# Performance work log

Measured on AMD Instinct MI355X. Metric: run time of the kernel, lower is better.

## Reference

```python
import jax, jax.numpy as jnp
import numpy as np

D_MODEL = 512
NUM_HEADS = 8
HEAD_DIM = D_MODEL // NUM_HEADS  # 64
EMBEDDING_DIM = 512  # undefined global EmbeddingDim in source -> d_model
EVENT_DIM = 388      # undefined global EventDim in source -> MIDI event vocab
B, T = 2, 2048


def setup_inputs() -> dict:
    key = jax.random.key(0)
    ks = jax.random.split(key, 12)
    sc = 0.02
    v = jax.random.normal(ks[0], (B, T, D_MODEL), jnp.float32)
    k = jax.random.normal(ks[1], (B, T, D_MODEL), jnp.float32)
    q = jax.random.normal(ks[2], (B, T, D_MODEL), jnp.float32)
    mask = jnp.tril(jnp.ones((T, T), jnp.float32))  # causal mask, broadcasts to [H,B,T,T]
    Wq = jax.random.normal(ks[3], (D_MODEL, HEAD_DIM), jnp.float32) * sc
    bq = jnp.zeros((HEAD_DIM,), jnp.float32)
    Wk = jax.random.normal(ks[4], (D_MODEL, HEAD_DIM), jnp.float32) * sc
    bk = jnp.zeros((HEAD_DIM,), jnp.float32)
    Wv = jax.random.normal(ks[5], (D_MODEL, HEAD_DIM), jnp.float32) * sc
    bv = jnp.zeros((HEAD_DIM,), jnp.float32)
    E = jax.random.normal(ks[6], (NUM_HEADS, T, HEAD_DIM), jnp.float32) * sc
    Wo = jax.random.normal(ks[7], (D_MODEL, EMBEDDING_DIM), jnp.float32) * sc
    bo = jnp.zeros((EMBEDDING_DIM,), jnp.float32)
    Wl = jax.random.normal(ks[8], (EMBEDDING_DIM, EVENT_DIM), jnp.float32) * sc
    bl = jnp.zeros((EVENT_DIM,), jnp.float32)
    return {"v": v, "k": k, "q": q, "mask": mask, "Wq": Wq, "bq": bq,
            "Wk": Wk, "bk": bk, "Wv": Wv, "bv": bv, "E": E,
            "Wo": Wo, "bo": bo, "Wl": Wl, "bl": bl}


def _skew(S):
    # S: [H,B,T,T] -> Music-Transformer skew via left-pad, reshape, slice
    H, Bb, Tt, _ = S.shape
    S = jnp.pad(S, ((0, 0), (0, 0), (0, 0), (1, 0)))          # [H,B,T,T+1]
    S = S.reshape(H, Bb, Tt + 1, Tt)                           # [H,B,T+1,T]
    return S[:, :, 1:]                                         # [H,B,T,T]


def reference(v, k, q, mask, Wq, bq, Wk, bk, Wv, bv, E, Wo, bo, Wl, bl):
    # The source applies the SAME Dense per head, so all heads share q/k/v projections
    qh = q @ Wq + bq  # [B,T,hd]
    kh = k @ Wk + bk  # [B,T,hd]
    vh = v @ Wv + bv  # [B,T,hd]
    # relative-position scores per head: Q @ E^T then skew
    S = jnp.einsum('btd,hsd->hbts', qh, E)  # [H,B,T,T]
    S = _skew(S)
    qk = jnp.einsum('btd,bsd->bts', qh, kh)  # [B,T,T], identical across heads
    attn = (qk[None] + S) / np.sqrt(HEAD_DIM)  # [H,B,T,T]
    attn = attn * mask - jnp.asarray(1e10, attn.dtype) * (1.0 - mask)
    score = jax.nn.softmax(attn, axis=-1)
    ctx = jnp.einsum('hbts,bsd->hbtd', score, vh)  # [H,B,T,hd]
    ctx = jnp.transpose(ctx, (1, 2, 0, 3)).reshape(ctx.shape[1], ctx.shape[2], -1)  # [B,T,d_model]
    ctx = jax.nn.relu(ctx @ Wo + bo)  # [B,T,EmbeddingDim]
    logits = ctx @ Wl + bl            # [B,T,EventDim]
    return logits
```

## Files before the change

### kernel.cpp

```cpp
#include <hip/hip_runtime.h>
#include <hip/hip_bf16.h>


#define B_ 2
#define T_ 2048
#define DM_ 512
#define H_ 8
#define HD_ 64
#define ED_ 512
#define EV_ 388
#define BT_ (B_ * T_)

typedef __attribute__((ext_vector_type(8))) short short8;
typedef __attribute__((ext_vector_type(4))) float floatx4;

#define MFMA(a, b, c) __builtin_amdgcn_mfma_f32_16x16x32_bf16((a), (b), (c), 0, 0, 0)

__device__ __forceinline__ float bfs(unsigned short s) {
  union { unsigned int i; float f; } v; v.i = ((unsigned int)s) << 16; return v.f;
}
__device__ __forceinline__ unsigned short f2bf(float f) {
  __hip_bfloat16 h = __float2bfloat16(f);
  union { __hip_bfloat16 h; unsigned short u; } v; v.h = h; return v.u;
}
__device__ __forceinline__ float ldf(const void* p, int i, bool isbf) {
  return isbf ? bfs(((const unsigned short*)p)[i]) : ((const float*)p)[i];
}
__device__ __forceinline__ bool det_bf(const unsigned int* mask) {
  return mask[0] != 0x3F800000u;
}

__global__ __launch_bounds__(256) void prep_kernel(
    const void* __restrict__ E, const void* __restrict__ Wq,
    const void* __restrict__ Wk, const void* __restrict__ Wv,
    const void* __restrict__ Wo, const void* __restrict__ Wl,
    const unsigned int* __restrict__ mask,
    unsigned short* __restrict__ E_c, unsigned short* __restrict__ WqT,
    unsigned short* __restrict__ WkT, unsigned short* __restrict__ WvT,
    unsigned short* __restrict__ WoT, unsigned short* __restrict__ WlT) {
  const bool isbf = det_bf(mask);
  const int tid = threadIdx.x;
  int bi = blockIdx.x;
  if (bi < 1024) {
    const int i0 = (bi * 256 + tid) * 4;
    if (isbf) {
      *(uint2*)&E_c[i0] = *(const uint2*)((const unsigned short*)E + i0);
    } else {
      float4 f = *(const float4*)((const float*)E + i0);
      unsigned short p[4] = {f2bf(f.x), f2bf(f.y), f2bf(f.z), f2bf(f.w)};
      *(uint2*)&E_c[i0] = *(uint2*)p;
    }
    return;
  }
  bi -= 1024;
  const void* src; unsigned short* dst; int N, nb;
  if (bi < 16)       { src = Wq; dst = WqT; N = 64;  nb = bi; }
  else if (bi < 32)  { src = Wk; dst = WkT; N = 64;  nb = bi - 16; }
  else if (bi < 48)  { src = Wv; dst = WvT; N = 64;  nb = bi - 32; }
  else if (bi < 176) { src = Wo; dst = WoT; N = 512; nb = bi - 48; }
  else               { src = Wl; dst = WlT; N = 388; nb = bi - 176; }
  const int n = nb * 4 + (tid >> 6);
  const int k0 = (tid & 63) * 8;
  unsigned short vv[8];
#pragma unroll
  for (int j = 0; j < 8; ++j) {
    if (n >= N) vv[j] = 0;
    else if (isbf) vv[j] = ((const unsigned short*)src)[(size_t)(k0 + j) * N + n];
    else vv[j] = f2bf(((const float*)src)[(size_t)(k0 + j) * N + n]);
  }
  *(uint4*)&dst[(size_t)n * DM_ + k0] = *(uint4*)vv;
}

__global__ __launch_bounds__(256) void gemm_proj(
    const void* __restrict__ xq, const void* __restrict__ xk,
    const void* __restrict__ xv,
    const unsigned short* __restrict__ WqT, const unsigned short* __restrict__ WkT,
    const unsigned short* __restrict__ WvT,
    const void* __restrict__ bq, const void* __restrict__ bk,
    const void* __restrict__ bv, const unsigned int* __restrict__ mask,
    unsigned short* __restrict__ oq, unsigned short* __restrict__ ok,
    unsigned short* __restrict__ ovt) {
  __shared__ __align__(16) short sA[64][72];
  __shared__ __align__(16) short sW[64][72];
  const int sel = blockIdx.y;
  const void* x = (sel == 0) ? xq : (sel == 1) ? xk : xv;
  const unsigned short* WT = (sel == 0) ? WqT : (sel == 1) ? WkT : WvT;
  const void* bias = (sel == 0) ? bq : (sel == 1) ? bk : bv;
  const bool isbf = det_bf(mask);

  const int tid = threadIdx.x;
  const int w = tid >> 6, lane = tid & 63;
  const int q_ = lane >> 4, n_ = lane & 15;
  const int row0 = blockIdx.x * 64;

  floatx4 acc[4];
#pragma unroll
  for (int j = 0; j < 4; ++j) acc[j] = (floatx4){0.f, 0.f, 0.f, 0.f};

  for (int k0 = 0; k0 < DM_; k0 += 64) {
    if (isbf) {
#pragma unroll
      for (int it = 0; it < 2; ++it) {
        int idx = tid + it * 256;
        int rr = idx >> 3, cc = (idx & 7) * 8;
        *(uint4*)&sA[rr][cc] =
            *(const uint4*)((const unsigned short*)x + (size_t)(row0 + rr) * DM_ + k0 + cc);
      }
    } else {
#pragma unroll
      for (int it = 0; it < 4; ++it) {
        int idx = tid + it * 256;
        int rr = idx >> 4, cc = (idx & 15) * 4;
        float4 f = *(const float4*)((const float*)x + (size_t)(row0 + rr) * DM_ + k0 + cc);
        unsigned short p[4] = {f2bf(f.x), f2bf(f.y), f2bf(f.z), f2bf(f.w)};
        *(uint2*)&sA[rr][cc] = *(uint2*)p;
      }
    }
#pragma unroll
    for (int it = 0; it < 2; ++it) {
      int idx = tid + it * 256;
      int rr = idx >> 3, cc = (idx & 7) * 8;
      *(uint4*)&sW[rr][cc] = *(const uint4*)(WT + (size_t)rr * DM_ + k0 + cc);
    }
    __syncthreads();
    short8 a0 = *(const short8*)&sA[16 * w + n_][8 * q_];
    short8 a1 = *(const short8*)&sA[16 * w + n_][32 + 8 * q_];
#pragma unroll
    for (int nb = 0; nb < 4; ++nb) {
      short8 b0 = *(const short8*)&sW[16 * nb + n_][8 * q_];
      short8 b1 = *(const short8*)&sW[16 * nb + n_][32 + 8 * q_];
      acc[nb] = MFMA(a0, b0, acc[nb]);
      acc[nb] = MFMA(a1, b1, acc[nb]);
    }
    __syncthreads();
  }

#pragma unroll
  for (int nb = 0; nb < 4; ++nb) {
    const int col = 16 * nb + n_;
    const float bb = ldf(bias, col, isbf);
#pragma unroll
    for (int r = 0; r < 4; ++r) {
      int row = row0 + 16 * w + 4 * q_ + r;
      unsigned short val = f2bf(acc[nb][r] + bb);
      if (sel < 2) {
        unsigned short* o = (sel == 0) ? oq : ok;
        o[(size_t)row * HD_ + col] = val;
      } else {
        int b = row >> 11, s = row & 2047;
        ovt[(((size_t)(b * HD_ + col)) << 11) + s] = val;
      }
    }
  }
}

__device__ __forceinline__ int pbase_of(int ti) {
  return (ti < 16) ? (ti - 8) * 2 : (ti < 24) ? 16 + (ti - 16) * 3
                                              : 40 + (ti - 24) * 4;
}

__global__ __launch_bounds__(256) void attn_kernel(
    const unsigned short* __restrict__ qh, const unsigned short* __restrict__ kh,
    const unsigned short* __restrict__ vt, const unsigned short* __restrict__ E,
    unsigned short* __restrict__ ctxo, float* __restrict__ pc,
    float* __restrict__ ml) {
  __shared__ __align__(16) short sK[64][72];
  __shared__ __align__(16) short sVT[64][72];
  __shared__ __align__(16) short sP[64][72];

  const int id = blockIdx.x;
  const int hb = id / 80;
  const int rem = id % 80;
  int ti, c, nc;
  if (rem < 8)       { ti = rem;                 c = 0;            nc = 1; }
  else if (rem < 24) { ti = 8 + ((rem - 8) >> 1);  c = (rem - 8) & 1;  nc = 2; }
  else if (rem < 48) { ti = 16 + (rem - 24) / 3;   c = (rem - 24) % 3; nc = 3; }
  else               { ti = 24 + ((rem - 48) >> 2); c = (rem - 48) & 3; nc = 4; }
  const int nsteps = ti + 1;
  const int klo = (c * nsteps) / nc;
  const int khi = ((c + 1) * nsteps) / nc;

  const int h = hb >> 1, b = hb & 1;
  const int t0 = ti * 64;

  const int tid = threadIdx.x;
  const int w = tid >> 6, lane = tid & 63;
  const int q_ = lane >> 4, n_ = lane & 15;

  const int trow = t0 + 16 * w + n_;
  const unsigned short* qp = qh + (((size_t)((b << 11) + trow)) << 6) + (q_ << 3);
  const short8 qa0 = *(const short8*)qp;
  const short8 qa1 = *(const short8*)(qp + 32);

  short8 onesf;
#pragma unroll
  for (int j = 0; j < 8; ++j) onesf[j] = (short)0x3F80;

  floatx4 ctxa[4];
#pragma unroll
  for (int nb = 0; nb < 4; ++nb) ctxa[nb] = (floatx4){0.f, 0.f, 0.f, 0.f};
  floatx4 lacc = (floatx4){0.f, 0.f, 0.f, 0.f};

  const unsigned short* eb = E + ((size_t)h << 17);
  const unsigned short* kbase = kh + (((size_t)(b << 11)) << 6);
  const unsigned short* vbase = vt + (((size_t)(b << 6)) << 11);
  const int rrS = tid >> 3, ccS = (tid & 7) * 8;

  for (int kt = klo; kt < khi; ++kt) {
    const int s0 = kt * 64;
    const int rb = (T_ - 64) + s0 - t0;

    short8 e0[5], e1[5];
#pragma unroll
    for (int f = 0; f < 5; ++f) {
      int gr = rb + 16 * (3 - w + f) + n_;
      if (gr > T_ - 1) gr = T_ - 1;
      const unsigned short* ep = eb + ((size_t)gr << 6) + (q_ << 3);
      e0[f] = *(const short8*)ep;
      e1[f] = *(const short8*)(ep + 32);
    }

    __syncthreads();
#pragma unroll
    for (int it = 0; it < 2; ++it) {
      int rr = rrS + it * 32;
      *(uint4*)&sK[rr][ccS] =
          *(const uint4*)(kbase + (((size_t)(s0 + rr)) << 6) + ccS);
      *(uint4*)&sVT[rr][ccS] =
          *(const uint4*)(vbase + (((size_t)rr) << 11) + s0 + ccS);
    }
    __syncthreads();

    floatx4 qk[4];
#pragma unroll
    for (int nb = 0; nb < 4; ++nb) {
      short8 kb0 = *(const short8*)&sK[16 * nb + n_][8 * q_];
      short8 kb1 = *(const short8*)&sK[16 * nb + n_][32 + 8 * q_];
      qk[nb] = (floatx4){0.f, 0.f, 0.f, 0.f};
      qk[nb] = MFMA(qa0, kb0, qk[nb]);
      qk[nb] = MFMA(qa1, kb1, qk[nb]);
    }
    floatx4 qe[5];
#pragma unroll
    for (int f = 0; f < 5; ++f) {
      qe[f] = (floatx4){0.f, 0.f, 0.f, 0.f};
      qe[f] = MFMA(qa0, e0[f], qe[f]);
      qe[f] = MFMA(qa1, e1[f], qe[f]);
    }

    const bool diag = (kt == ti);
#pragma unroll
    for (int r = 0; r < 4; ++r) {
      const int t = 4 * q_ + r;
      const int ba = ((q_ << 4) | ((n_ - t + 15) & 15)) << 2;
      const int nd = (n_ + t + 1) & 15;
      const bool hi = nd > t;
#pragma unroll
      for (int mb = 0; mb < 4; ++mb) {
        float merged = hi ? qe[mb + 1][r] : qe[mb][r];
        float g = __int_as_float(
            __builtin_amdgcn_ds_bpermute(ba, __float_as_int(merged)));
        float sv = (qk[mb][r] + g) * 0.125f;
        if (diag && (16 * mb + n_ > 16 * w + t)) sv = -1.0e30f;
        sP[16 * w + t][16 * mb + n_] = (short)f2bf(__expf(sv));
      }
    }

    short8 pa0 = *(const short8*)&sP[16 * w + n_][8 * q_];
    short8 pa1 = *(const short8*)&sP[16 * w + n_][32 + 8 * q_];
#pragma unroll
    for (int nb = 0; nb < 4; ++nb) {
      short8 v0 = *(const short8*)&sVT[16 * nb + n_][8 * q_];
      short8 v1 = *(const short8*)&sVT[16 * nb + n_][32 + 8 * q_];
      ctxa[nb] = MFMA(pa0, v0, ctxa[nb]);
      ctxa[nb] = MFMA(pa1, v1, ctxa[nb]);
    }
    lacc = MFMA(pa0, onesf, lacc);
    lacc = MFMA(pa1, onesf, lacc);
  }

  if (nc == 1) {
#pragma unroll
    for (int r = 0; r < 4; ++r) {
      const float inv = 1.0f / lacc[r];
      const int row = t0 + 16 * w + 4 * q_ + r;
      const size_t base = (((size_t)((b << 11) + row)) << 9) + (h << 6) + n_;
#pragma unroll
      for (int nb = 0; nb < 4; ++nb)
        ctxo[base + 16 * nb] = f2bf(ctxa[nb][r] * inv);
    }
  } else {
    const int idx = hb * 72 + pbase_of(ti) + c;
    float* pcb = pc + ((size_t)idx << 12);
    float* mlb = ml + ((size_t)idx << 6);
#pragma unroll
    for (int r = 0; r < 4; ++r) {
      const int row = 16 * w + 4 * q_ + r;
#pragma unroll
      for (int nb = 0; nb < 4; ++nb)
        pcb[(row << 6) + 16 * nb + n_] = ctxa[nb][r];
      if (n_ == 0) mlb[row] = lacc[r];
    }
  }
}

__global__ __launch_bounds__(256) void combine_kernel(
    const float* __restrict__ pc, const float* __restrict__ ml,
    unsigned short* __restrict__ ctxo) {
  const int cb = blockIdx.x;
  const int hb = cb / 24;
  const int ti = 8 + cb % 24;
  const int nc = (ti >> 3) + 1;
  const int h = hb >> 1, b = hb & 1, t0 = ti * 64;
  const int tid = threadIdx.x;
  const int row = tid >> 2, seg = (tid & 3) * 16;
  const int idx0 = hb * 72 + pbase_of(ti);

  float lsum = 0.f;
  float4 a4[4];
#pragma unroll
  for (int j = 0; j < 4; ++j) a4[j] = (float4){0.f, 0.f, 0.f, 0.f};
  for (int c = 0; c < nc; ++c) {
    const int idx = idx0 + c;
    lsum += ml[((size_t)idx << 6) + row];
    const float* cp = pc + ((size_t)idx << 12) + (row << 6) + seg;
#pragma unroll
    for (int j = 0; j < 4; ++j) {
      float4 x = *(const float4*)(cp + 4 * j);
      a4[j].x += x.x; a4[j].y += x.y; a4[j].z += x.z; a4[j].w += x.w;
    }
  }
  const float inv = 1.0f / lsum;
  unsigned short o[16];
#pragma unroll
  for (int j = 0; j < 4; ++j) {
    o[4 * j + 0] = f2bf(a4[j].x * inv);
    o[4 * j + 1] = f2bf(a4[j].y * inv);
    o[4 * j + 2] = f2bf(a4[j].z * inv);
    o[4 * j + 3] = f2bf(a4[j].w * inv);
  }
  unsigned short* dst =
      ctxo + (((size_t)((b << 11) + t0 + row)) << 9) + (h << 6) + seg;
  *(uint4*)dst = *(uint4*)&o[0];
  *(uint4*)(dst + 8) = *(uint4*)&o[8];
}

template <int RELU>
__global__ __launch_bounds__(256) void mlp_mfma(
    const unsigned short* __restrict__ A, const unsigned short* __restrict__ WT,
    const void* __restrict__ bias, unsigned short* __restrict__ outBF,
    void* __restrict__ outD, const unsigned int* __restrict__ mask) {
  __shared__ __align__(16) short sA[64][72];
  __shared__ __align__(16) short sW[64][72];
  const int tid = threadIdx.x;
  const int w = tid >> 6, lane = tid & 63;
  const int q_ = lane >> 4, n_ = lane & 15;
  const int row0 = blockIdx.x * 64;
  const int n0 = blockIdx.y * 64;
  const bool isbf = det_bf(mask);

  floatx4 acc[4];
#pragma unroll
  for (int j = 0; j < 4; ++j) acc[j] = (floatx4){0.f, 0.f, 0.f, 0.f};

  for (int k0 = 0; k0 < DM_; k0 += 64) {
#pragma unroll
    for (int it = 0; it < 2; ++it) {
      int idx = tid + it * 256;
      int rr = idx >> 3, cc = (idx & 7) * 8;
      *(uint4*)&sA[rr][cc] = *(const uint4*)(A + (size_t)(row0 + rr) * DM_ + k0 + cc);
      *(uint4*)&sW[rr][cc] = *(const uint4*)(WT + (size_t)(n0 + rr) * DM_ + k0 + cc);
    }
    __syncthreads();
    short8 a0 = *(const short8*)&sA[16 * w + n_][8 * q_];
    short8 a1 = *(const short8*)&sA[16 * w + n_][32 + 8 * q_];
#pragma unroll
    for (int nb = 0; nb < 4; ++nb) {
      short8 b0 = *(const short8*)&sW[16 * nb + n_][8 * q_];
      short8 b1 = *(const short8*)&sW[16 * nb + n_][32 + 8 * q_];
      acc[nb] = MFMA(a0, b0, acc[nb]);
      acc[nb] = MFMA(a1, b1, acc[nb]);
    }
    __syncthreads();
  }

#pragma unroll
  for (int nb = 0; nb < 4; ++nb) {
    const int col = n0 + 16 * nb + n_;
    float bb = 0.f;
    if (RELU || col < EV_) bb = ldf(bias, col, isbf);
#pragma unroll
    for (int r = 0; r < 4; ++r) {
      const int row = row0 + 16 * w + 4 * q_ + r;
      float v = acc[nb][r] + bb;
      if (RELU) {
        outBF[(size_t)row * ED_ + col] = f2bf(fmaxf(v, 0.f));
      } else if (col < EV_) {
        if (isbf) ((unsigned short*)outD)[(size_t)row * EV_ + col] = f2bf(v);
        else      ((float*)outD)[(size_t)row * EV_ + col] = v;
      }
    }
  }
}

extern "C" void kernel_launch(void* const* d_in, const int* in_sizes, int n_in,
                              void* d_out, int out_size, void* d_ws, size_t ws_size,
                              hipStream_t stream) {
  const void* v  = d_in[0];
  const void* k  = d_in[1];
  const void* q  = d_in[2];
  const unsigned int* mask = (const unsigned int*)d_in[3];
  const void* Wq = d_in[4];
  const void* bq = d_in[5];
  const void* Wk = d_in[6];
  const void* bk = d_in[7];
  const void* Wv = d_in[8];
  const void* bv = d_in[9];
  const void* E  = d_in[10];
  const void* Wo = d_in[11];
  const void* bo = d_in[12];
  const void* Wl = d_in[13];
  const void* bl = d_in[14];

  char* p = (char*)d_ws;
  unsigned short* E_c  = (unsigned short*)p; p += (size_t)H_ * T_ * HD_ * 2;
  unsigned short* qhb  = (unsigned short*)p; p += (size_t)BT_ * HD_ * 2;
  unsigned short* khb  = (unsigned short*)p; p += (size_t)BT_ * HD_ * 2;
  unsigned short* vtb  = (unsigned short*)p; p += (size_t)BT_ * HD_ * 2;
  unsigned short* WqT  = (unsigned short*)p; p += (size_t)HD_ * DM_ * 2;
  unsigned short* WkT  = (unsigned short*)p; p += (size_t)HD_ * DM_ * 2;
  unsigned short* WvT  = (unsigned short*)p; p += (size_t)HD_ * DM_ * 2;
  unsigned short* WoT  = (unsigned short*)p; p += (size_t)ED_ * DM_ * 2;
  unsigned short* WlT  = (unsigned short*)p; p += (size_t)448 * DM_ * 2;
  unsigned short* ctxb = (unsigned short*)p; p += (size_t)BT_ * DM_ * 2;
  unsigned short* h1b  = (unsigned short*)p; p += (size_t)BT_ * ED_ * 2;
  float* pc = (float*)p; p += (size_t)16 * 72 * 4096 * 4;
  float* ml = (float*)p; p += (size_t)16 * 72 * 64 * 4;

  prep_kernel<<<dim3(1312), 256, 0, stream>>>(
      E, Wq, Wk, Wv, Wo, Wl, mask, E_c, WqT, WkT, WvT, WoT, WlT);
  gemm_proj<<<dim3(BT_ / 64, 3), 256, 0, stream>>>(
      q, k, v, WqT, WkT, WvT, bq, bk, bv, mask, qhb, khb, vtb);
  attn_kernel<<<dim3(1280), 256, 0, stream>>>(qhb, khb, vtb, E_c, ctxb, pc, ml);
  combine_kernel<<<dim3(384), 256, 0, stream>>>(pc, ml, ctxb);
  mlp_mfma<1><<<dim3(BT_ / 64, ED_ / 64), 256, 0, stream>>>(
      ctxb, WoT, bo, h1b, nullptr, mask);
  mlp_mfma<0><<<dim3(BT_ / 64, 448 / 64), 256, 0, stream>>>(
      h1b, WlT, bl, nullptr, d_out, mask);
}
```

Baseline: 225.0 us.

## Double-buffer K/V tiles in attention and fold split-KV combine via atomic counter

The attention loop now prefetches the next K/V tile into registers while computing on the current one, using double-buffered shared memory to hide global load latency. The separate combine kernel is removed: each split block bumps an atomic counter, and the last block to finish for a query tile reduces the partial results and writes the context. The counters are zeroed inside the projection kernel. This saves one kernel launch and overlaps memory with compute, at the cost of more shared memory, more register pressure and extra fences and atomics.

```diff
diff --git a/kernel.cpp b/kernel.cpp
--- a/kernel.cpp
+++ b/kernel.cpp
@@ -79,16 +79,19 @@
     const void* __restrict__ bq, const void* __restrict__ bk,
     const void* __restrict__ bv, const unsigned int* __restrict__ mask,
     unsigned short* __restrict__ oq, unsigned short* __restrict__ ok,
-    unsigned short* __restrict__ ovt) {
+    unsigned short* __restrict__ ovt, int* __restrict__ cnt) {
   __shared__ __align__(16) short sA[64][72];
   __shared__ __align__(16) short sW[64][72];
+  const int tid = threadIdx.x;
+  if (blockIdx.x == 0 && blockIdx.y == 0 && tid < 128) {
+    cnt[tid] = 0; cnt[tid + 128] = 0; cnt[tid + 256] = 0;
+  }
   const int sel = blockIdx.y;
   const void* x = (sel == 0) ? xq : (sel == 1) ? xk : xv;
   const unsigned short* WT = (sel == 0) ? WqT : (sel == 1) ? WkT : WvT;
   const void* bias = (sel == 0) ? bq : (sel == 1) ? bk : bv;
   const bool isbf = det_bf(mask);
 
-  const int tid = threadIdx.x;
   const int w = tid >> 6, lane = tid & 63;
   const int q_ = lane >> 4, n_ = lane & 15;
   const int row0 = blockIdx.x * 64;
@@ -163,16 +166,17 @@
     const unsigned short* __restrict__ qh, const unsigned short* __restrict__ kh,
     const unsigned short* __restrict__ vt, const unsigned short* __restrict__ E,
     unsigned short* __restrict__ ctxo, float* __restrict__ pc,
-    float* __restrict__ ml) {
-  __shared__ __align__(16) short sK[64][72];
-  __shared__ __align__(16) short sVT[64][72];
+    float* __restrict__ ml, int* __restrict__ cnt) {
+  __shared__ __align__(16) short sK[2][64][72];
+  __shared__ __align__(16) short sVT[2][64][72];
   __shared__ __align__(16) short sP[64][72];
+  __shared__ int lastFlag;
 
   const int id = blockIdx.x;
   const int hb = id / 80;
   const int rem = id % 80;
   int ti, c, nc;
-  if (rem < 8)       { ti = rem;                 c = 0;            nc = 1; }
+  if (rem < 8)       { ti = rem;                  c = 0;             nc = 1; }
   else if (rem < 24) { ti = 8 + ((rem - 8) >> 1);  c = (rem - 8) & 1;  nc = 2; }
   else if (rem < 48) { ti = 16 + (rem - 24) / 3;   c = (rem - 24) % 3; nc = 3; }
   else               { ti = 24 + ((rem - 48) >> 2); c = (rem - 48) & 3; nc = 4; }
@@ -206,9 +210,32 @@
   const unsigned short* vbase = vt + (((size_t)(b << 6)) << 11);
   const int rrS = tid >> 3, ccS = (tid & 7) * 8;
 
+  uint4 pk[2], pv[2];
+#define LOADKV(KT)                                                            \
+  {                                                                           \
+    const int s0p = (KT) * 64;                                                \
+    _Pragma("unroll")                                                         \
+    for (int it = 0; it < 2; ++it) {                                          \
+      int rr = rrS + it * 32;                                                 \
+      pk[it] = *(const uint4*)(kbase + (((size_t)(s0p + rr)) << 6) + ccS);    \
+      pv[it] = *(const uint4*)(vbase + (((size_t)rr) << 11) + s0p + ccS);     \
+    }                                                                         \
+  }
+
+  LOADKV(klo);
+#pragma unroll
+  for (int it = 0; it < 2; ++it) {
+    int rr = rrS + it * 32;
+    *(uint4*)&sK[0][rr][ccS] = pk[it];
+    *(uint4*)&sVT[0][rr][ccS] = pv[it];
+  }
+  __syncthreads();
+
+  int cur = 0;
   for (int kt = klo; kt < khi; ++kt) {
     const int s0 = kt * 64;
     const int rb = (T_ - 64) + s0 - t0;
+    const bool hasNext = (kt + 1 < khi);
 
     short8 e0[5], e1[5];
 #pragma unroll
@@ -219,23 +246,13 @@
       e0[f] = *(const short8*)ep;
       e1[f] = *(const short8*)(ep + 32);
     }
-
-    __syncthreads();
-#pragma unroll
-    for (int it = 0; it < 2; ++it) {
-      int rr = rrS + it * 32;
-      *(uint4*)&sK[rr][ccS] =
-          *(const uint4*)(kbase + (((size_t)(s0 + rr)) << 6) + ccS);
-      *(uint4*)&sVT[rr][ccS] =
-          *(const uint4*)(vbase + (((size_t)rr) << 11) + s0 + ccS);
-    }
-    __syncthreads();
+    if (hasNext) LOADKV(kt + 1);
 
     floatx4 qk[4];
 #pragma unroll
     for (int nb = 0; nb < 4; ++nb) {
-      short8 kb0 = *(const short8*)&sK[16 * nb + n_][8 * q_];
-      short8 kb1 = *(const short8*)&sK[16 * nb + n_][32 + 8 * q_];
+      short8 kb0 = *(const short8*)&sK[cur][16 * nb + n_][8 * q_];
+      short8 kb1 = *(const short8*)&sK[cur][16 * nb + n_][32 + 8 * q_];
       qk[nb] = (floatx4){0.f, 0.f, 0.f, 0.f};
       qk[nb] = MFMA(qa0, kb0, qk[nb]);
       qk[nb] = MFMA(qa1, kb1, qk[nb]);
@@ -270,14 +287,27 @@
     short8 pa1 = *(const short8*)&sP[16 * w + n_][32 + 8 * q_];
 #pragma unroll
     for (int nb = 0; nb < 4; ++nb) {
-      short8 v0 = *(const short8*)&sVT[16 * nb + n_][8 * q_];
-      short8 v1 = *(const short8*)&sVT[16 * nb + n_][32 + 8 * q_];
+      short8 v0 = *(const short8*)&sVT[cur][16 * nb + n_][8 * q_];
+      short8 v1 = *(const short8*)&sVT[cur][16 * nb + n_][32 + 8 * q_];
       ctxa[nb] = MFMA(pa0, v0, ctxa[nb]);
       ctxa[nb] = MFMA(pa1, v1, ctxa[nb]);
     }
     lacc = MFMA(pa0, onesf, lacc);
     lacc = MFMA(pa1, onesf, lacc);
-  }
+
+    if (hasNext) {
+      __syncthreads();
+#pragma unroll
+      for (int it = 0; it < 2; ++it) {
+        int rr = rrS + it * 32;
+        *(uint4*)&sK[cur ^ 1][rr][ccS] = pk[it];
+        *(uint4*)&sVT[cur ^ 1][rr][ccS] = pv[it];
+      }
+      __syncthreads();
+      cur ^= 1;
+    }
+  }
+#undef LOADKV
 
   if (nc == 1) {
 #pragma unroll
@@ -301,48 +331,45 @@
         pcb[(row << 6) + 16 * nb + n_] = ctxa[nb][r];
       if (n_ == 0) mlb[row] = lacc[r];
     }
-  }
-}
-
-__global__ __launch_bounds__(256) void combine_kernel(
-    const float* __restrict__ pc, const float* __restrict__ ml,
-    unsigned short* __restrict__ ctxo) {
-  const int cb = blockIdx.x;
-  const int hb = cb / 24;
-  const int ti = 8 + cb % 24;
-  const int nc = (ti >> 3) + 1;
-  const int h = hb >> 1, b = hb & 1, t0 = ti * 64;
-  const int tid = threadIdx.x;
-  const int row = tid >> 2, seg = (tid & 3) * 16;
-  const int idx0 = hb * 72 + pbase_of(ti);
-
-  float lsum = 0.f;
-  float4 a4[4];
-#pragma unroll
-  for (int j = 0; j < 4; ++j) a4[j] = (float4){0.f, 0.f, 0.f, 0.f};
-  for (int c = 0; c < nc; ++c) {
-    const int idx = idx0 + c;
-    lsum += ml[((size_t)idx << 6) + row];
-    const float* cp = pc + ((size_t)idx << 12) + (row << 6) + seg;
-#pragma unroll
-    for (int j = 0; j < 4; ++j) {
-      float4 x = *(const float4*)(cp + 4 * j);
-      a4[j].x += x.x; a4[j].y += x.y; a4[j].z += x.z; a4[j].w += x.w;
-    }
-  }
-  const float inv = 1.0f / lsum;
-  unsigned short o[16];
-#pragma unroll
-  for (int j = 0; j < 4; ++j) {
-    o[4 * j + 0] = f2bf(a4[j].x * inv);
-    o[4 * j + 1] = f2bf(a4[j].y * inv);
-    o[4 * j + 2] = f2bf(a4[j].z * inv);
-    o[4 * j + 3] = f2bf(a4[j].w * inv);
-  }
-  unsigned short* dst =
-      ctxo + (((size_t)((b << 11) + t0 + row)) << 9) + (h << 6) + seg;
-  *(uint4*)dst = *(uint4*)&o[0];
-  *(uint4*)(dst + 8) = *(uint4*)&o[8];
+    __threadfence();
+    if (tid == 0) {
+      int old = atomicAdd(&cnt[hb * 24 + (ti - 8)], 1);
+      lastFlag = (old == nc - 1) ? 1 : 0;
+    }
+    __syncthreads();
+    if (lastFlag) {
+      __threadfence();
+      const int row = tid >> 2, seg = (tid & 3) * 16;
+      const int idx0 = hb * 72 + pbase_of(ti);
+      float lsum = 0.f;
+      float4 a4[4];
+#pragma unroll
+      for (int j = 0; j < 4; ++j) a4[j] = (float4){0.f, 0.f, 0.f, 0.f};
+      for (int c2 = 0; c2 < nc; ++c2) {
+        const int ix = idx0 + c2;
+        lsum += ml[((size_t)ix << 6) + row];
+        const float* cp = pc + ((size_t)ix << 12) + (row << 6) + seg;
+#pragma unroll
+        for (int j = 0; j < 4; ++j) {
+          float4 x = *(const float4*)(cp + 4 * j);
+          a4[j].x += x.x; a4[j].y += x.y; a4[j].z += x.z; a4[j].w += x.w;
+        }
+      }
+      const float inv = 1.0f / lsum;
+      unsigned short o[16];
+#pragma unroll
+      for (int j = 0; j < 4; ++j) {
+        o[4 * j + 0] = f2bf(a4[j].x * inv);
+        o[4 * j + 1] = f2bf(a4[j].y * inv);
+        o[4 * j + 2] = f2bf(a4[j].z * inv);
+        o[4 * j + 3] = f2bf(a4[j].w * inv);
+      }
+      unsigned short* dst =
+          ctxo + (((size_t)((b << 11) + t0 + row)) << 9) + (h << 6) + seg;
+      *(uint4*)dst = *(uint4*)&o[0];
+      *(uint4*)(dst + 8) = *(uint4*)&o[8];
+    }
+  }
 }
 
 template <int RELU>
@@ -436,13 +463,14 @@
   unsigned short* h1b  = (unsigned short*)p; p += (size_t)BT_ * ED_ * 2;
   float* pc = (float*)p; p += (size_t)16 * 72 * 4096 * 4;
   float* ml = (float*)p; p += (size_t)16 * 72 * 64 * 4;
+  int* cnt = (int*)p;    p += 384 * 4;
 
   prep_kernel<<<dim3(1312), 256, 0, stream>>>(
       E, Wq, Wk, Wv, Wo, Wl, mask, E_c, WqT, WkT, WvT, WoT, WlT);
   gemm_proj<<<dim3(BT_ / 64, 3), 256, 0, stream>>>(
-      q, k, v, WqT, WkT, WvT, bq, bk, bv, mask, qhb, khb, vtb);
-  attn_kernel<<<dim3(1280), 256, 0, stream>>>(qhb, khb, vtb, E_c, ctxb, pc, ml);
-  combine_kernel<<<dim3(384), 256, 0, stream>>>(pc, ml, ctxb);
+      q, k, v, WqT, WkT, WvT, bq, bk, bv, mask, qhb, khb, vtb, cnt);
+  attn_kernel<<<dim3(1280), 256, 0, stream>>>(
+      qhb, khb, vtb, E_c, ctxb, pc, ml, cnt);
   mlp_mfma<1><<<dim3(BT_ / 64, ED_ / 64), 256, 0, stream>>>(
       ctxb, WoT, bo, h1b, nullptr, mask);
   mlp_mfma<0><<<dim3(BT_ / 64, 448 / 64), 256, 0, stream>>>(
```

Result: slower. 485.7 us (+115.9%).

## Prefetch next K/V tile into registers and load MLP operands directly from global

Applied to the files above, without the earlier changes.

In the attention kernel, the next K and V^T tile is loaded from global memory into registers while the current tile is being computed, then written to shared memory at the end of the iteration. This hides global load latency behind the MFMA work. Separately, the MLP GEMM kernel drops its shared-memory staging and has each wave read its A and W fragments straight from global memory, removing two barriers per k-step. The cost is that W fragments are re-read by all four waves through cache, and the extra prefetch registers may reduce occupancy.

```diff
diff --git a/kernel.cpp b/kernel.cpp
--- a/kernel.cpp
+++ b/kernel.cpp
@@ -172,7 +172,7 @@
   const int hb = id / 80;
   const int rem = id % 80;
   int ti, c, nc;
-  if (rem < 8)       { ti = rem;                 c = 0;            nc = 1; }
+  if (rem < 8)       { ti = rem;                  c = 0;             nc = 1; }
   else if (rem < 24) { ti = 8 + ((rem - 8) >> 1);  c = (rem - 8) & 1;  nc = 2; }
   else if (rem < 48) { ti = 16 + (rem - 24) / 3;   c = (rem - 24) % 3; nc = 3; }
   else               { ti = 24 + ((rem - 48) >> 2); c = (rem - 48) & 3; nc = 4; }
@@ -206,9 +206,31 @@
   const unsigned short* vbase = vt + (((size_t)(b << 6)) << 11);
   const int rrS = tid >> 3, ccS = (tid & 7) * 8;
 
+  uint4 pk[2], pv[2];
+#define LOADKV(KT)                                                            \
+  {                                                                           \
+    const int s0p = (KT) * 64;                                                \
+    _Pragma("unroll")                                                         \
+    for (int it = 0; it < 2; ++it) {                                          \
+      int rr = rrS + it * 32;                                                 \
+      pk[it] = *(const uint4*)(kbase + (((size_t)(s0p + rr)) << 6) + ccS);    \
+      pv[it] = *(const uint4*)(vbase + (((size_t)rr) << 11) + s0p + ccS);     \
+    }                                                                         \
+  }
+
+  LOADKV(klo);
+#pragma unroll
+  for (int it = 0; it < 2; ++it) {
+    int rr = rrS + it * 32;
+    *(uint4*)&sK[rr][ccS] = pk[it];
+    *(uint4*)&sVT[rr][ccS] = pv[it];
+  }
+  __syncthreads();
+
   for (int kt = klo; kt < khi; ++kt) {
     const int s0 = kt * 64;
     const int rb = (T_ - 64) + s0 - t0;
+    const bool hasNext = (kt + 1 < khi);
 
     short8 e0[5], e1[5];
 #pragma unroll
@@ -219,17 +241,7 @@
       e0[f] = *(const short8*)ep;
       e1[f] = *(const short8*)(ep + 32);
     }
-
-    __syncthreads();
-#pragma unroll
-    for (int it = 0; it < 2; ++it) {
-      int rr = rrS + it * 32;
-      *(uint4*)&sK[rr][ccS] =
-          *(const uint4*)(kbase + (((size_t)(s0 + rr)) << 6) + ccS);
-      *(uint4*)&sVT[rr][ccS] =
-          *(const uint4*)(vbase + (((size_t)rr) << 11) + s0 + ccS);
-    }
-    __syncthreads();
+    if (hasNext) LOADKV(kt + 1);
 
     floatx4 qk[4];
 #pragma unroll
@@ -277,7 +289,19 @@
     }
     lacc = MFMA(pa0, onesf, lacc);
     lacc = MFMA(pa1, onesf, lacc);
-  }
+
+    if (hasNext) {
+      __syncthreads();
+#pragma unroll
+      for (int it = 0; it < 2; ++it) {
+        int rr = rrS + it * 32;
+        *(uint4*)&sK[rr][ccS] = pk[it];
+        *(uint4*)&sVT[rr][ccS] = pv[it];
+      }
+      __syncthreads();
+    }
+  }
+#undef LOADKV
 
   if (nc == 1) {
 #pragma unroll
@@ -350,8 +374,6 @@
     const unsigned short* __restrict__ A, const unsigned short* __restrict__ WT,
     const void* __restrict__ bias, unsigned short* __restrict__ outBF,
     void* __restrict__ outD, const unsigned int* __restrict__ mask) {
-  __shared__ __align__(16) short sA[64][72];
-  __shared__ __align__(16) short sW[64][72];
   const int tid = threadIdx.x;
   const int w = tid >> 6, lane = tid & 63;
   const int q_ = lane >> 4, n_ = lane & 15;
@@ -359,29 +381,29 @@
   const int n0 = blockIdx.y * 64;
   const bool isbf = det_bf(mask);
 
+  const unsigned short* arow = A + (size_t)(row0 + 16 * w + n_) * DM_ + 8 * q_;
+  const unsigned short* wrow = WT + (size_t)(n0 + n_) * DM_ + 8 * q_;
+
   floatx4 acc[4];
 #pragma unroll
   for (int j = 0; j < 4; ++j) acc[j] = (floatx4){0.f, 0.f, 0.f, 0.f};
 
+#pragma unroll 2
   for (int k0 = 0; k0 < DM_; k0 += 64) {
-#pragma unroll
-    for (int it = 0; it < 2; ++it) {
-      int idx = tid + it * 256;
-      int rr = idx >> 3, cc = (idx & 7) * 8;
-      *(uint4*)&sA[rr][cc] = *(const uint4*)(A + (size_t)(row0 + rr) * DM_ + k0 + cc);
-      *(uint4*)&sW[rr][cc] = *(const uint4*)(WT + (size_t)(n0 + rr) * DM_ + k0 + cc);
-    }
-    __syncthreads();
-    short8 a0 = *(const short8*)&sA[16 * w + n_][8 * q_];
-    short8 a1 = *(const short8*)&sA[16 * w + n_][32 + 8 * q_];
+    short8 a0 = *(const short8*)(arow + k0);
+    short8 a1 = *(const short8*)(arow + k0 + 32);
+    short8 b0[4], b1[4];
 #pragma unroll
     for (int nb = 0; nb < 4; ++nb) {
-      short8 b0 = *(const short8*)&sW[16 * nb + n_][8 * q_];
-      short8 b1 = *(const short8*)&sW[16 * nb + n_][32 + 8 * q_];
-      acc[nb] = MFMA(a0, b0, acc[nb]);
-      acc[nb] = MFMA(a1, b1, acc[nb]);
-    }
-    __syncthreads();
+      const unsigned short* wp = wrow + ((size_t)(16 * nb) << 9) + k0;
+      b0[nb] = *(const short8*)wp;
+      b1[nb] = *(const short8*)(wp + 32);
+    }
+#pragma unroll
+    for (int nb = 0; nb < 4; ++nb) {
+      acc[nb] = MFMA(a0, b0[nb], acc[nb]);
+      acc[nb] = MFMA(a1, b1[nb], acc[nb]);
+    }
   }
 
 #pragma unroll
```

Measured after the change: 267.1 us. 1.19x slower.
